# Kernel optimization log

Measured on AMD Instinct MI355X. Metric: run time of the kernel, lower is better.

## Reference

```python
import jax, jax.numpy as jnp
import numpy as np

N_NODES = 100000
N_GRAPHS = 256
EPS = 1e-5


def setup_inputs() -> dict:
    key = jax.random.key(0)
    ks = jax.random.split(key, 16)
    x = jax.random.normal(ks[0], (N_NODES, 7), dtype=jnp.float32)
    edge_index = jax.random.randint(ks[1], (2, 1600000), 0, N_NODES, dtype=jnp.int64)
    batch = jnp.sort(jax.random.randint(ks[2], (N_NODES,), 0, N_GRAPHS, dtype=jnp.int64))

    def lin(k, fi, fo):
        s = 1.0 / np.sqrt(fi)
        kw, kb = jax.random.split(k)
        W = jax.random.uniform(kw, (fi, fo), jnp.float32, -s, s)
        b = jax.random.uniform(kb, (fo,), jnp.float32, -s, s)
        return W, b

    W1, b1 = lin(ks[3], 7, 71)
    W2, b2 = lin(ks[4], 71, 135)
    W3, b3 = lin(ks[5], 135, 199)
    Wl1, bl1 = lin(ks[6], 199, 49)
    Wl2, bl2 = lin(ks[7], 49, 2)
    return {
        "x": x, "edge_index": edge_index, "batch": batch,
        "bn0_g": jnp.ones((7,)), "bn0_b": jnp.zeros((7,)),
        "bn1_g": jnp.ones((71,)), "bn1_b": jnp.zeros((71,)),
        "bn2_g": jnp.ones((135,)), "bn2_b": jnp.zeros((135,)),
        "W1": W1, "b1": b1, "W2": W2, "b2": b2, "W3": W3, "b3": b3,
        "Wl1": Wl1, "bl1": bl1, "Wl2": Wl2, "bl2": bl2,
    }


def _bn(x, g, b):
    # BatchNorm1d in training mode: batch stats over node dim
    m = jnp.mean(x, axis=0)
    v = jnp.mean(jnp.square(x - m), axis=0)
    return (x - m) * jax.lax.rsqrt(v + EPS) * g + b


def _gcn(x, src, dst, norm, W, b):
    # PyG GCNConv: x' = D^{-1/2} (A+I) D^{-1/2} (x W) + b
    h = x @ W
    out = jax.ops.segment_sum(norm[:, None] * h[src], dst, num_segments=N_NODES)
    return out + b


def reference(x, edge_index, batch, bn0_g, bn0_b, bn1_g, bn1_b, bn2_g, bn2_b,
              W1, b1, W2, b2, W3, b3, Wl1, bl1, Wl2, bl2):
    # add self loops
    loops = jnp.arange(N_NODES, dtype=edge_index.dtype)
    src = jnp.concatenate([edge_index[0], loops])
    dst = jnp.concatenate([edge_index[1], loops])
    deg = jax.ops.segment_sum(jnp.ones_like(dst, dtype=x.dtype), dst, num_segments=N_NODES)
    d_isqrt = jax.lax.rsqrt(jnp.maximum(deg, 1.0))
    norm = d_isqrt[src] * d_isqrt[dst]

    h = _bn(x, bn0_g, bn0_b)
    h = jax.nn.relu(_gcn(h, src, dst, norm, W1, b1))
    h = _bn(h, bn1_g, bn1_b)
    h = jax.nn.relu(_gcn(h, src, dst, norm, W2, b2))
    h = _bn(h, bn2_g, bn2_b)
    h = jax.nn.relu(_gcn(h, src, dst, norm, W3, b3))

    # global mean pool over graphs
    sums = jax.ops.segment_sum(h, batch, num_segments=N_GRAPHS)
    cnts = jax.ops.segment_sum(jnp.ones((h.shape[0],), h.dtype), batch, num_segments=N_GRAPHS)
    pooled = sums / jnp.maximum(cnts, 1.0)[:, None]

    out = pooled @ Wl1 + bl1
    out = out @ Wl2 + bl2
    return out
```

## Files before the change

### kernel.cpp

```cpp
#include <hip/hip_runtime.h>
#include <hip/hip_fp16.h>

#define EPSV 1e-5f
#define BIN_CH 4096
#define BCAP 8192

typedef _Float16 f16;
typedef f16 half8 __attribute__((ext_vector_type(8)));
typedef float f32x4 __attribute__((ext_vector_type(4)));


__global__ __launch_bounds__(256) void k_bin(const int* __restrict__ src,
                                             const int* __restrict__ dst, int E, int EN,
                                             int NBK, int* __restrict__ gcur,
                                             int* __restrict__ binned) {
    __shared__ int cnt[512];
    __shared__ int base[512];
    for (int b = threadIdx.x; b < 512; b += 256) cnt[b] = 0;
    __syncthreads();
    int i0 = blockIdx.x * BIN_CH;
    int i1 = i0 + BIN_CH; if (i1 > EN) i1 = EN;
    for (int i = i0 + threadIdx.x; i < i1; i += 256) {
        int d = (i < E) ? dst[i] : (i - E);
        atomicAdd(&cnt[d >> 8], 1);
    }
    __syncthreads();
    for (int b = threadIdx.x; b < NBK; b += 256)
        if (cnt[b]) base[b] = b * BCAP + atomicAdd(&gcur[b], cnt[b]);
    __syncthreads();
    for (int i = i0 + threadIdx.x; i < i1; i += 256) {
        int s, d;
        if (i < E) { s = src[i]; d = dst[i]; }
        else       { s = i - E; d = s; }
        int pos = atomicAdd(&base[d >> 8], 1);
        binned[pos] = s | ((d & 255) << 24);
    }
}

__global__ __launch_bounds__(256) void k_bucket(const int* __restrict__ binned,
                                                const int* __restrict__ gcur, int N,
                                                int* __restrict__ deg, int* __restrict__ rs,
                                                int* __restrict__ csr_s,
                                                float* __restrict__ disq) {
    __shared__ int deg_l[256];
    __shared__ int sc[256];
    __shared__ int cur_l[256];
    int b = blockIdx.x;
    int t = threadIdx.x;
    int start = b * BCAP, end = start + gcur[b];
    deg_l[t] = 0;
    __syncthreads();
    for (int i = start + t; i < end; i += 256)
        atomicAdd(&deg_l[((unsigned)binned[i]) >> 24], 1);
    __syncthreads();
    sc[t] = deg_l[t];
    __syncthreads();
    for (int off = 1; off < 256; off <<= 1) {
        int v = (t >= off) ? sc[t - off] : 0;
        __syncthreads();
        sc[t] += v;
        __syncthreads();
    }
    int rs_l = sc[t] - deg_l[t];
    int n = b * 256 + t;
    if (n < N) {
        deg[n] = deg_l[t];
        rs[n] = start + rs_l;
        disq[n] = rsqrtf((float)(deg_l[t] > 0 ? deg_l[t] : 1));
    }
    cur_l[t] = start + rs_l;
    __syncthreads();
    for (int i = start + t; i < end; i += 256) {
        int p = binned[i];
        int loc = ((unsigned)p) >> 24;
        int idx = atomicAdd(&cur_l[loc], 1);
        csr_s[idx] = p & 0xFFFFFF;
    }
}

__global__ __launch_bounds__(256) void k_wfill(const int* __restrict__ rs,
                                               const int* __restrict__ deg,
                                               const int* __restrict__ csr_s,
                                               const float* __restrict__ disq,
                                               float* __restrict__ csr_w, int N) {
    int wave = threadIdx.x >> 6, lane = threadIdx.x & 63;
    int n = blockIdx.x * 4 + wave;
    if (n >= N) return;
    int e0 = rs[n], dg = deg[n];
    float dn = disq[n];
    for (int j = lane; j < dg; j += 64) {
        int s = csr_s[e0 + j];
        csr_w[e0 + j] = disq[s] * dn;
    }
}


__global__ __launch_bounds__(256) void k_prep(
    const float* __restrict__ colsum, const float* __restrict__ colsq,
    const float* __restrict__ g, const float* __restrict__ b, float invN,
    const float* __restrict__ W, int Cin, int Cout, int KP,
    f16* __restrict__ Wp, float* __restrict__ wrow) {
    __shared__ float lsc[192];
    __shared__ float lsh[192];
    __shared__ float red[4];
    int t = threadIdx.x;
    int c = blockIdx.x;
    if (t < KP) {
        float scv = 0.f, shv = 0.f;
        if (t < Cin) {
            float m = colsum[t] * invN;
            float v = colsq[t] * invN - m * m;
            float rstd = rsqrtf(fmaxf(v, 0.f) + EPSV);
            scv = rstd * g[t];
            shv = b[t] - m * scv;
        }
        lsc[t] = scv; lsh[t] = shv;
    }
    __syncthreads();
    float part = 0.f;
    if (t < KP) {
        float wv = (t < Cin && c < Cout) ? W[(size_t)t * Cout + c] : 0.f;
        Wp[(size_t)c * KP + t] = (f16)(lsc[t] * wv);
        part = lsh[t] * wv;
    }
    for (int off = 32; off > 0; off >>= 1) part += __shfl_down(part, off);
    int lane = t & 63, wid = t >> 6;
    if (lane == 0) red[wid] = part;
    __syncthreads();
    if (t == 0) wrow[c] = red[0] + red[1] + red[2] + red[3];
}


__global__ __launch_bounds__(256) void k_padx_stats(const float* __restrict__ x,
                                                    __half* __restrict__ xp, int N,
                                                    float* __restrict__ colsum,
                                                    float* __restrict__ colsq) {
    __shared__ float ls[16];
    int t = threadIdx.x;
    int n = blockIdx.x * 256 + t;
    int lane = t & 63;
    if (t < 16) ls[t] = 0.f;
    __syncthreads();
    float v[7] = {0.f, 0.f, 0.f, 0.f, 0.f, 0.f, 0.f};
    if (n < N) {
#pragma unroll
        for (int j = 0; j < 7; ++j) v[j] = x[(size_t)n * 7 + j];
        __half h[8];
#pragma unroll
        for (int j = 0; j < 7; ++j) h[j] = __float2half(v[j]);
        h[7] = __float2half(0.f);
        *(float4*)(xp + (size_t)n * 8) = *(float4*)h;
    }
#pragma unroll
    for (int j = 0; j < 7; ++j) {
        float s = v[j];
        float q = v[j] * v[j];
        for (int off = 32; off > 0; off >>= 1) {
            s += __shfl_down(s, off);
            q += __shfl_down(q, off);
        }
        if (lane == 0) {
            atomicAdd(&ls[j], s);
            atomicAdd(&ls[8 + j], q);
        }
    }
    __syncthreads();
    if (t < 8)               atomicAdd(&colsum[t], ls[t]);
    else if (t < 16)         atomicAdd(&colsq[t - 8], ls[t]);
}


__global__ void k_gather8(const __half* __restrict__ xp, const int* __restrict__ csr_s,
                          const float* __restrict__ csr_w,
                          const int* __restrict__ rs, const int* __restrict__ deg,
                          __half* __restrict__ out, float* __restrict__ rsum, int N) {
    int n = blockIdx.x * blockDim.x + threadIdx.x;
    if (n >= N) return;
    int e0 = rs[n], eend = e0 + deg[n];
    float a0 = 0.f, a1 = 0.f, a2 = 0.f, a3 = 0.f, a4 = 0.f, a5 = 0.f, a6 = 0.f, a7 = 0.f;
    float ws = 0.f;
    for (int e = e0; e < eend; ++e) {
        int s = csr_s[e];
        float w = csr_w[e];
        ws += w;
        float4 r = *(const float4*)(xp + (size_t)s * 8);
        const __half2* hh = (const __half2*)&r;
        float2 q0 = __half22float2(hh[0]);
        float2 q1 = __half22float2(hh[1]);
        float2 q2 = __half22float2(hh[2]);
        float2 q3 = __half22float2(hh[3]);
        a0 = fmaf(w, q0.x, a0); a1 = fmaf(w, q0.y, a1);
        a2 = fmaf(w, q1.x, a2); a3 = fmaf(w, q1.y, a3);
        a4 = fmaf(w, q2.x, a4); a5 = fmaf(w, q2.y, a5);
        a6 = fmaf(w, q3.x, a6); a7 = fmaf(w, q3.y, a7);
    }
    rsum[n] = ws;
    __half h[8];
    h[0] = __float2half(a0); h[1] = __float2half(a1);
    h[2] = __float2half(a2); h[3] = __float2half(a3);
    h[4] = __float2half(a4); h[5] = __float2half(a5);
    h[6] = __float2half(a6); h[7] = __float2half(a7);
    *(float4*)(out + (size_t)n * 8) = *(float4*)h;
}

__global__ __launch_bounds__(256) void k_gather_w(
    const __half* __restrict__ Am, int SPm, const __half* __restrict__ At,
    int CH8, int NPW,
    const int* __restrict__ rs, const int* __restrict__ deg,
    const int* __restrict__ csr_s, const float* __restrict__ csr_w,
    __half* __restrict__ out, int SPo, int N) {
    int wave = threadIdx.x >> 6;
    int lane = threadIdx.x & 63;
    int sub = lane / CH8;
    int lsub = lane - sub * CH8;
    int n = (blockIdx.x * 4 + wave) * NPW + sub;
    bool active = (sub < NPW) && (n < N);
    int e0 = 0, eend = 0;
    if (active) { e0 = rs[n]; eend = e0 + deg[n]; }
    bool istail = (lsub == CH8 - 1);
    const __half* base = istail ? At : (Am + lsub * 8);
    const int stride = istail ? 8 : SPm;
    float acc[8] = {};

    int e = e0;
    for (; e + 8 <= eend; e += 8) {
        int s[8]; float wv[8]; float4 r[8];
#pragma unroll
        for (int i = 0; i < 8; ++i) { s[i] = csr_s[e + i]; wv[i] = csr_w[e + i]; }
#pragma unroll
        for (int i = 0; i < 8; ++i) r[i] = *(const float4*)(base + (size_t)(s[i] * stride));
#pragma unroll
        for (int i = 0; i < 8; ++i) {
            float2 q0 = __half22float2(((const __half2*)&r[i])[0]);
            float2 q1 = __half22float2(((const __half2*)&r[i])[1]);
            float2 q2 = __half22float2(((const __half2*)&r[i])[2]);
            float2 q3 = __half22float2(((const __half2*)&r[i])[3]);
            acc[0] = fmaf(wv[i], q0.x, acc[0]); acc[1] = fmaf(wv[i], q0.y, acc[1]);
            acc[2] = fmaf(wv[i], q1.x, acc[2]); acc[3] = fmaf(wv[i], q1.y, acc[3]);
            acc[4] = fmaf(wv[i], q2.x, acc[4]); acc[5] = fmaf(wv[i], q2.y, acc[5]);
            acc[6] = fmaf(wv[i], q3.x, acc[6]); acc[7] = fmaf(wv[i], q3.y, acc[7]);
        }
    }
    for (; e + 4 <= eend; e += 4) {
        int s[4]; float wv[4]; float4 r[4];
#pragma unroll
        for (int i = 0; i < 4; ++i) { s[i] = csr_s[e + i]; wv[i] = csr_w[e + i]; }
#pragma unroll
        for (int i = 0; i < 4; ++i) r[i] = *(const float4*)(base + (size_t)(s[i] * stride));
#pragma unroll
        for (int i = 0; i < 4; ++i) {
            float2 q0 = __half22float2(((const __half2*)&r[i])[0]);
            float2 q1 = __half22float2(((const __half2*)&r[i])[1]);
            float2 q2 = __half22float2(((const __half2*)&r[i])[2]);
            float2 q3 = __half22float2(((const __half2*)&r[i])[3]);
            acc[0] = fmaf(wv[i], q0.x, acc[0]); acc[1] = fmaf(wv[i], q0.y, acc[1]);
            acc[2] = fmaf(wv[i], q1.x, acc[2]); acc[3] = fmaf(wv[i], q1.y, acc[3]);
            acc[4] = fmaf(wv[i], q2.x, acc[4]); acc[5] = fmaf(wv[i], q2.y, acc[5]);
            acc[6] = fmaf(wv[i], q3.x, acc[6]); acc[7] = fmaf(wv[i], q3.y, acc[7]);
        }
    }
    for (; e < eend; ++e) {
        int s = csr_s[e];
        float w = csr_w[e];
        float4 r = *(const float4*)(base + (size_t)(s * stride));
        float2 q0 = __half22float2(((const __half2*)&r)[0]);
        float2 q1 = __half22float2(((const __half2*)&r)[1]);
        float2 q2 = __half22float2(((const __half2*)&r)[2]);
        float2 q3 = __half22float2(((const __half2*)&r)[3]);
        acc[0] = fmaf(w, q0.x, acc[0]); acc[1] = fmaf(w, q0.y, acc[1]);
        acc[2] = fmaf(w, q1.x, acc[2]); acc[3] = fmaf(w, q1.y, acc[3]);
        acc[4] = fmaf(w, q2.x, acc[4]); acc[5] = fmaf(w, q2.y, acc[5]);
        acc[6] = fmaf(w, q3.x, acc[6]); acc[7] = fmaf(w, q3.y, acc[7]);
    }

    if (active) {
        __half2 h[4];
        h[0] = __floats2half2_rn(acc[0], acc[1]);
        h[1] = __floats2half2_rn(acc[2], acc[3]);
        h[2] = __floats2half2_rn(acc[4], acc[5]);
        h[3] = __floats2half2_rn(acc[6], acc[7]);
        *(float4*)(out + (size_t)n * SPo + lsub * 8) = *(float4*)h;
    }
}


__global__ __launch_bounds__(256) void k_gemm_mfma(
    const f16* __restrict__ A, int SPa,
    const f16* __restrict__ Bt, int KP,
    const float* __restrict__ rsum, const float* __restrict__ wrow,
    const float* __restrict__ bias,
    f16* __restrict__ outM, int SPm, int MAIN, f16* __restrict__ outT, int TOTW,
    float* __restrict__ colsum, float* __restrict__ colsq, int do_stats,
    int N, int Cout) {
    __shared__ f16 As[128][40];
    __shared__ float s_sum[64];
    __shared__ float s_sq[64];
    const int r0 = blockIdx.x * 128;
    const int c0 = blockIdx.y * 64;
    const int t = threadIdx.x;
    const int wave = t >> 6, lane = t & 63;
    const int l15 = lane & 15, quad = lane >> 4;

    if (t < 64) { s_sum[t] = 0.f; s_sq[t] = 0.f; }

    f32x4 zero4 = {0.f, 0.f, 0.f, 0.f};
    f32x4 acc[2][4];
#pragma unroll
    for (int mi = 0; mi < 2; ++mi)
#pragma unroll
        for (int ni = 0; ni < 4; ++ni) acc[mi][ni] = zero4;

    const int KT = KP >> 5;
    for (int kt = 0; kt < KT; ++kt) {
        int k0 = kt * 32;
        {
            int kcol = (t & 7) * 4;
            int rbase = t >> 3;
            int gk = k0 + kcol;
            bool kok = (gk + 4 <= SPa);
#pragma unroll
            for (int i = 0; i < 4; ++i) {
                int row = rbase + i * 32;
                int gr = r0 + row;
                ushort4 v = {0, 0, 0, 0};
                if (gr < N && kok)
                    v = *(const ushort4*)(A + (size_t)gr * SPa + gk);
                *(ushort4*)&As[row][kcol] = v;
            }
        }
        __syncthreads();
        half8 a0 = *(const half8*)&As[wave * 32 + l15][quad * 8];
        half8 a1 = *(const half8*)&As[wave * 32 + 16 + l15][quad * 8];
#pragma unroll
        for (int ni = 0; ni < 4; ++ni) {
            half8 b = *(const half8*)(Bt + (size_t)(c0 + ni * 16 + l15) * KP + k0 + quad * 8);
            acc[0][ni] = __builtin_amdgcn_mfma_f32_16x16x32_f16(a0, b, acc[0][ni], 0, 0, 0);
            acc[1][ni] = __builtin_amdgcn_mfma_f32_16x16x32_f16(a1, b, acc[1][ni], 0, 0, 0);
        }
        __syncthreads();
    }

    float wr[4], bi[4];
#pragma unroll
    for (int ni = 0; ni < 4; ++ni) {
        int gc = c0 + ni * 16 + l15;
        wr[ni] = wrow[gc];
        bi[ni] = (gc < Cout) ? bias[gc] : 0.f;
    }
    float ps[4] = {}, pq[4] = {};
#pragma unroll
    for (int mi = 0; mi < 2; ++mi) {
#pragma unroll
        for (int reg = 0; reg < 4; ++reg) {
            int gr = r0 + wave * 32 + mi * 16 + quad * 4 + reg;
            if (gr >= N) continue;
            float rsv = rsum[gr];
#pragma unroll
            for (int ni = 0; ni < 4; ++ni) {
                int gc = c0 + ni * 16 + l15;
                float o = acc[mi][ni][reg] + rsv * wr[ni] + bi[ni];
                o = fmaxf(o, 0.f);
                if (gc >= Cout) o = 0.f;
                ps[ni] += o; pq[ni] += o * o;
                if (gc < MAIN) {
                    if (gc < TOTW) outM[(size_t)gr * SPm + gc] = (f16)o;
                } else if (gc < TOTW) {
                    outT[(size_t)gr * 8 + (gc - MAIN)] = (f16)o;
                }
            }
        }
    }
    if (do_stats) {
#pragma unroll
        for (int ni = 0; ni < 4; ++ni) {
            int cl = ni * 16 + l15;
            atomicAdd(&s_sum[cl], ps[ni]);
            atomicAdd(&s_sq[cl], pq[ni]);
        }
        __syncthreads();
        if (t < 64 && c0 + t < Cout) {
            atomicAdd(&colsum[c0 + t], s_sum[t]);
            atomicAdd(&colsq[c0 + t], s_sq[t]);
        }
    }
}


__global__ void k_pool_h(const __half* __restrict__ H, int SP, const int* __restrict__ batch,
                         int N, int C, float* __restrict__ pooled,
                         int* __restrict__ gstart, int* __restrict__ gend) {
    __shared__ int sb[128];
    int r0 = blockIdx.x * 128;
    int rows = N - r0; if (rows > 128) rows = 128;
    int t = threadIdx.x;
    if (t < rows) sb[t] = batch[r0 + t];
    __syncthreads();
    if (t < rows) {
        int n = r0 + t, g = sb[t];
        int prev = (n == 0) ? -1 : ((t == 0) ? batch[n - 1] : sb[t - 1]);
        if (prev != g) gstart[g] = n;
        int nxt = (n == N - 1) ? -1 : ((t == rows - 1) ? batch[n + 1] : sb[t + 1]);
        if (nxt != g) gend[g] = n + 1;
    }
    int c = t;
    if (c >= C) return;
    int cg = sb[0];
    float acc = 0.f;
    for (int r = 0; r < rows; ++r) {
        int g = sb[r];
        if (g != cg) { atomicAdd(&pooled[cg * C + c], acc); acc = 0.f; cg = g; }
        acc += __half2float(H[(size_t)(r0 + r) * SP + c]);
    }
    atomicAdd(&pooled[cg * C + c], acc);
}


__global__ void k_mlp(const float* __restrict__ pooled, const int* __restrict__ gstart,
                      const int* __restrict__ gend,
                      const float* __restrict__ Wl1, const float* __restrict__ bl1,
                      const float* __restrict__ Wl2, const float* __restrict__ bl2,
                      float* __restrict__ out, int C) {
    __shared__ float p[199];
    __shared__ float t1[49];
    int g = blockIdx.x;
    int cnt = gend[g] - gstart[g];
    float inv = 1.f / (float)(cnt > 1 ? cnt : 1);
    for (int k = threadIdx.x; k < C; k += blockDim.x) p[k] = pooled[g * C + k] * inv;
    __syncthreads();
    if (threadIdx.x < 49) {
        float acc = bl1[threadIdx.x];
        for (int k = 0; k < C; ++k) acc += p[k] * Wl1[k * 49 + threadIdx.x];
        t1[threadIdx.x] = acc;
    }
    __syncthreads();
    if (threadIdx.x < 2) {
        float acc = bl2[threadIdx.x];
        for (int k = 0; k < 49; ++k) acc += t1[k] * Wl2[k * 2 + threadIdx.x];
        out[g * 2 + threadIdx.x] = acc;
    }
}


extern "C" void kernel_launch(void* const* d_in, const int* in_sizes, int n_in,
                              void* d_out, int out_size, void* d_ws, size_t ws_size,
                              hipStream_t stream) {
    const float* x     = (const float*)d_in[0];
    const int*   ei    = (const int*)d_in[1];
    const int*   batch = (const int*)d_in[2];
    const float* bn0g = (const float*)d_in[3];
    const float* bn0b = (const float*)d_in[4];
    const float* bn1g = (const float*)d_in[5];
    const float* bn1b = (const float*)d_in[6];
    const float* bn2g = (const float*)d_in[7];
    const float* bn2b = (const float*)d_in[8];
    const float* W1  = (const float*)d_in[9];
    const float* b1  = (const float*)d_in[10];
    const float* W2  = (const float*)d_in[11];
    const float* b2  = (const float*)d_in[12];
    const float* W3  = (const float*)d_in[13];
    const float* b3  = (const float*)d_in[14];
    const float* Wl1 = (const float*)d_in[15];
    const float* bl1 = (const float*)d_in[16];
    const float* Wl2 = (const float*)d_in[17];
    const float* bl2 = (const float*)d_in[18];

    const int N = in_sizes[0] / 7;
    const int E = in_sizes[1] / 2;
    const int EN = E + N;
    const int G = out_size / 2;
    const int NB = (N + 255) / 256;
    const int NBK = (N + 255) / 256;
    const int NBIN = (EN + BIN_CH - 1) / BIN_CH;

    const int* src = ei;
    const int* dst = ei + E;

    char* w = (char*)d_ws;
    auto alloc = [&](size_t bytes) -> void* {
        void* p = (void*)w;
        w += ((bytes + 255) / 256) * 256;
        return p;
    };
    size_t szH1m = (size_t)N * 64 * sizeof(__half);
    size_t szH1t = (size_t)N * 8 * sizeof(__half);
    size_t szH2m = (size_t)N * 128 * sizeof(__half);
    size_t szH2t = (size_t)N * 8 * sizeof(__half);
    char* regA = (char*)alloc(szH1m + szH1t + szH2m + szH2t);
    __half* H1m = (__half*)regA;
    __half* H1t = (__half*)(regA + szH1m);
    __half* H2m = (__half*)(regA + szH1m + szH1t);
    __half* H2t = (__half*)(regA + szH1m + szH1t + szH2m);
    __half* H3  = (__half*)regA;

    __half* bufG = (__half*)alloc((size_t)N * 136 * sizeof(__half));
    f16*    wp   = (f16*)  alloc((size_t)256 * 160 * sizeof(f16));
    float*  wrow = (float*)alloc(256 * sizeof(float));
    __half* xp   = (__half*)alloc((size_t)N * 8 * sizeof(__half));
    float* disq  = (float*)alloc((size_t)N * sizeof(float));
    float* rsum  = (float*)alloc((size_t)N * sizeof(float));
    int*   deg   = (int*)  alloc((size_t)N * sizeof(int));
    int*   rs    = (int*)  alloc((size_t)N * sizeof(int));
    int*   binned= (int*)  alloc((size_t)NBK * BCAP * sizeof(int));
    int*   csr_s = (int*)  alloc((size_t)NBK * BCAP * sizeof(int));
    float* csr_w = (float*)alloc((size_t)NBK * BCAP * sizeof(float));
    float* colsum0 = (float*)alloc(256 * sizeof(float));
    float* colsq0  = (float*)alloc(256 * sizeof(float));
    float* colsumA = (float*)alloc(256 * sizeof(float));
    float* colsqA  = (float*)alloc(256 * sizeof(float));
    float* colsumB = (float*)alloc(256 * sizeof(float));
    float* colsqB  = (float*)alloc(256 * sizeof(float));
    int*   gcur    = (int*)  alloc(512 * sizeof(int));
    float* pooled  = (float*)alloc((size_t)G * 199 * sizeof(float));
    int*   gstart  = (int*)  alloc((size_t)G * sizeof(int));
    int*   gend    = (int*)  alloc((size_t)G * sizeof(int));

    size_t zbytes = 6 * 1024 + 2048 + (((size_t)G * 199 * sizeof(float) + 255) / 256) * 256;
    hipMemsetAsync(colsum0, 0, zbytes, stream);

    k_bin<<<NBIN, 256, 0, stream>>>(src, dst, E, EN, NBK, gcur, binned);
    k_bucket<<<NBK, 256, 0, stream>>>(binned, gcur, N, deg, rs, csr_s, disq);
    k_wfill<<<(N + 3) / 4, 256, 0, stream>>>(rs, deg, csr_s, disq, csr_w, N);

    const int GB = (N + 127) / 128;

    k_padx_stats<<<NB, 256, 0, stream>>>(x, xp, N, colsum0, colsq0);
    k_prep<<<128, 256, 0, stream>>>(colsum0, colsq0, bn0g, bn0b, 1.f / (float)N,
                                    W1, 7, 71, 32, wp, wrow);
    k_gather8<<<(N + 255) / 256, 256, 0, stream>>>(xp, csr_s, csr_w, rs, deg, bufG, rsum, N);
    {
        dim3 grid(GB, 2);
        k_gemm_mfma<<<grid, 256, 0, stream>>>((const f16*)bufG, 8, wp, 32, rsum, wrow, b1,
                                              (f16*)H1m, 64, 64, (f16*)H1t, 72,
                                              colsumA, colsqA, 1, N, 71);
    }
    k_prep<<<192, 256, 0, stream>>>(colsumA, colsqA, bn1g, bn1b, 1.f / (float)N,
                                    W2, 71, 135, 96, wp, wrow);
    k_gather_w<<<(N + 27) / 28, 256, 0, stream>>>(H1m, 64, H1t, 9, 7,
                                                  rs, deg, csr_s, csr_w, bufG, 72, N);
    {
        dim3 grid(GB, 3);
        k_gemm_mfma<<<grid, 256, 0, stream>>>((const f16*)bufG, 72, wp, 96, rsum, wrow, b2,
                                              (f16*)H2m, 128, 128, (f16*)H2t, 136,
                                              colsumB, colsqB, 1, N, 135);
    }
    k_prep<<<256, 256, 0, stream>>>(colsumB, colsqB, bn2g, bn2b, 1.f / (float)N,
                                    W3, 135, 199, 160, wp, wrow);
    k_gather_w<<<(N + 11) / 12, 256, 0, stream>>>(H2m, 128, H2t, 17, 3,
                                                  rs, deg, csr_s, csr_w, bufG, 136, N);
    {
        dim3 grid(GB, 4);
        k_gemm_mfma<<<grid, 256, 0, stream>>>((const f16*)bufG, 136, wp, 160, rsum, wrow, b3,
                                              (f16*)H3, 200, 256, (f16*)nullptr, 200,
                                              colsumB, colsqB, 0, N, 199);
    }

    k_pool_h<<<(N + 127) / 128, 256, 0, stream>>>(H3, 200, batch, N, 199, pooled, gstart, gend);
    k_mlp<<<G, 64, 0, stream>>>(pooled, gstart, gend, Wl1, bl1, Wl2, bl2, (float*)d_out, 199);
}
```

Before: 530.9 us.

## Fuse final GCN GEMM with mean pooling and split tail gather into separate kernel

The last GEMM now writes its ReLU outputs straight into per-graph pooled sums, using shared-memory accumulation for up to 16 graphs per tile. This removes the H3 store and the separate pooling kernel. The graph start/end detection moves into the input stats kernel. The gather kernel drops its divergent tail-lane path so lanes map by power-of-two shifts, and the 8-channel tail columns are handled by a new per-node kernel. The cost is an extra launch per layer and atomic contention in the pooling epilogue.

Result: slower. 600.4 us (+13.1%).

```diff
diff --git a/kernel.cpp b/kernel.cpp
--- a/kernel.cpp
+++ b/kernel.cpp
@@ -134,7 +134,10 @@
 __global__ __launch_bounds__(256) void k_padx_stats(const float* __restrict__ x,
                                                     __half* __restrict__ xp, int N,
                                                     float* __restrict__ colsum,
-                                                    float* __restrict__ colsq) {
+                                                    float* __restrict__ colsq,
+                                                    const int* __restrict__ batch,
+                                                    int* __restrict__ gstart,
+                                                    int* __restrict__ gend) {
     __shared__ float ls[16];
     int t = threadIdx.x;
     int n = blockIdx.x * 256 + t;
@@ -150,6 +153,11 @@
         for (int j = 0; j < 7; ++j) h[j] = __float2half(v[j]);
         h[7] = __float2half(0.f);
         *(float4*)(xp + (size_t)n * 8) = *(float4*)h;
+        int g = batch[n];
+        int gp = (n == 0) ? -1 : batch[n - 1];
+        if (gp != g) gstart[g] = n;
+        int gn = (n == N - 1) ? -1 : batch[n + 1];
+        if (gn != g) gend[g] = n + 1;
     }
 #pragma unroll
     for (int j = 0; j < 7; ++j) {
@@ -203,23 +211,51 @@
     *(float4*)(out + (size_t)n * 8) = *(float4*)h;
 }
 
+__global__ __launch_bounds__(256) void k_gather_tail(
+    const __half* __restrict__ At, const int* __restrict__ csr_s,
+    const float* __restrict__ csr_w, const int* __restrict__ rs,
+    const int* __restrict__ deg, __half* __restrict__ out, int SPo, int coff, int N) {
+    int n = blockIdx.x * blockDim.x + threadIdx.x;
+    if (n >= N) return;
+    int e0 = rs[n], eend = e0 + deg[n];
+    float a0 = 0.f, a1 = 0.f, a2 = 0.f, a3 = 0.f, a4 = 0.f, a5 = 0.f, a6 = 0.f, a7 = 0.f;
+    for (int e = e0; e < eend; ++e) {
+        int s = csr_s[e];
+        float w = csr_w[e];
+        float4 r = *(const float4*)(At + (size_t)s * 8);
+        const __half2* hh = (const __half2*)&r;
+        float2 q0 = __half22float2(hh[0]);
+        float2 q1 = __half22float2(hh[1]);
+        float2 q2 = __half22float2(hh[2]);
+        float2 q3 = __half22float2(hh[3]);
+        a0 = fmaf(w, q0.x, a0); a1 = fmaf(w, q0.y, a1);
+        a2 = fmaf(w, q1.x, a2); a3 = fmaf(w, q1.y, a3);
+        a4 = fmaf(w, q2.x, a4); a5 = fmaf(w, q2.y, a5);
+        a6 = fmaf(w, q3.x, a6); a7 = fmaf(w, q3.y, a7);
+    }
+    __half2 h[4];
+    h[0] = __floats2half2_rn(a0, a1);
+    h[1] = __floats2half2_rn(a2, a3);
+    h[2] = __floats2half2_rn(a4, a5);
+    h[3] = __floats2half2_rn(a6, a7);
+    *(float4*)(out + (size_t)n * SPo + coff) = *(float4*)h;
+}
+
 __global__ __launch_bounds__(256) void k_gather_w(
-    const __half* __restrict__ Am, int SPm, const __half* __restrict__ At,
-    int CH8, int NPW,
+    const __half* __restrict__ Am, int SPm, int SH,
     const int* __restrict__ rs, const int* __restrict__ deg,
     const int* __restrict__ csr_s, const float* __restrict__ csr_w,
     __half* __restrict__ out, int SPo, int N) {
     int wave = threadIdx.x >> 6;
     int lane = threadIdx.x & 63;
-    int sub = lane / CH8;
-    int lsub = lane - sub * CH8;
-    int n = (blockIdx.x * 4 + wave) * NPW + sub;
-    bool active = (sub < NPW) && (n < N);
+    int sub = lane >> SH;
+    int lsub = lane & ((1 << SH) - 1);
+    int npw = 64 >> SH;
+    int n = (blockIdx.x * 4 + wave) * npw + sub;
+    bool active = (n < N);
     int e0 = 0, eend = 0;
     if (active) { e0 = rs[n]; eend = e0 + deg[n]; }
-    bool istail = (lsub == CH8 - 1);
-    const __half* base = istail ? At : (Am + lsub * 8);
-    const int stride = istail ? 8 : SPm;
+    const __half* base = Am + lsub * 8;
     float acc[8] = {};
 
     int e = e0;
@@ -228,7 +264,7 @@
 #pragma unroll
         for (int i = 0; i < 8; ++i) { s[i] = csr_s[e + i]; wv[i] = csr_w[e + i]; }
 #pragma unroll
-        for (int i = 0; i < 8; ++i) r[i] = *(const float4*)(base + (size_t)(s[i] * stride));
+        for (int i = 0; i < 8; ++i) r[i] = *(const float4*)(base + (size_t)s[i] * SPm);
 #pragma unroll
         for (int i = 0; i < 8; ++i) {
             float2 q0 = __half22float2(((const __half2*)&r[i])[0]);
@@ -246,7 +282,7 @@
 #pragma unroll
         for (int i = 0; i < 4; ++i) { s[i] = csr_s[e + i]; wv[i] = csr_w[e + i]; }
 #pragma unroll
-        for (int i = 0; i < 4; ++i) r[i] = *(const float4*)(base + (size_t)(s[i] * stride));
+        for (int i = 0; i < 4; ++i) r[i] = *(const float4*)(base + (size_t)s[i] * SPm);
 #pragma unroll
         for (int i = 0; i < 4; ++i) {
             float2 q0 = __half22float2(((const __half2*)&r[i])[0]);
@@ -262,7 +298,7 @@
     for (; e < eend; ++e) {
         int s = csr_s[e];
         float w = csr_w[e];
-        float4 r = *(const float4*)(base + (size_t)(s * stride));
+        float4 r = *(const float4*)(base + (size_t)s * SPm);
         float2 q0 = __half22float2(((const __half2*)&r)[0]);
         float2 q1 = __half22float2(((const __half2*)&r)[1]);
         float2 q2 = __half22float2(((const __half2*)&r)[2]);
@@ -386,32 +422,106 @@
 }
 
 
-__global__ void k_pool_h(const __half* __restrict__ H, int SP, const int* __restrict__ batch,
-                         int N, int C, float* __restrict__ pooled,
-                         int* __restrict__ gstart, int* __restrict__ gend) {
-    __shared__ int sb[128];
-    int r0 = blockIdx.x * 128;
-    int rows = N - r0; if (rows > 128) rows = 128;
-    int t = threadIdx.x;
-    if (t < rows) sb[t] = batch[r0 + t];
-    __syncthreads();
-    if (t < rows) {
-        int n = r0 + t, g = sb[t];
-        int prev = (n == 0) ? -1 : ((t == 0) ? batch[n - 1] : sb[t - 1]);
-        if (prev != g) gstart[g] = n;
-        int nxt = (n == N - 1) ? -1 : ((t == rows - 1) ? batch[n + 1] : sb[t + 1]);
-        if (nxt != g) gend[g] = n + 1;
-    }
-    int c = t;
-    if (c >= C) return;
-    int cg = sb[0];
-    float acc = 0.f;
-    for (int r = 0; r < rows; ++r) {
-        int g = sb[r];
-        if (g != cg) { atomicAdd(&pooled[cg * C + c], acc); acc = 0.f; cg = g; }
-        acc += __half2float(H[(size_t)(r0 + r) * SP + c]);
-    }
-    atomicAdd(&pooled[cg * C + c], acc);
+__global__ __launch_bounds__(256) void k_gemm_pool(
+    const f16* __restrict__ A, int SPa,
+    const f16* __restrict__ Bt, int KP,
+    const float* __restrict__ rsum, const float* __restrict__ wrow,
+    const float* __restrict__ bias, const int* __restrict__ batch,
+    float* __restrict__ pooled, int N, int Cout) {
+    __shared__ f16 As[128][40];
+    __shared__ int sbat[128];
+    __shared__ float s_pool[16][64];
+    const int r0 = blockIdx.x * 128;
+    const int c0 = blockIdx.y * 64;
+    const int t = threadIdx.x;
+    const int wave = t >> 6, lane = t & 63;
+    const int l15 = lane & 15, quad = lane >> 4;
+
+    if (t < 128) {
+        int gr = r0 + t;
+        sbat[t] = batch[(gr < N) ? gr : (N - 1)];
+    }
+    for (int i = t; i < 16 * 64; i += 256) ((float*)s_pool)[i] = 0.f;
+
+    f32x4 zero4 = {0.f, 0.f, 0.f, 0.f};
+    f32x4 acc[2][4];
+#pragma unroll
+    for (int mi = 0; mi < 2; ++mi)
+#pragma unroll
+        for (int ni = 0; ni < 4; ++ni) acc[mi][ni] = zero4;
+
+    const int KT = KP >> 5;
+    for (int kt = 0; kt < KT; ++kt) {
+        int k0 = kt * 32;
+        {
+            int kcol = (t & 7) * 4;
+            int rbase = t >> 3;
+            int gk = k0 + kcol;
+            bool kok = (gk + 4 <= SPa);
+#pragma unroll
+            for (int i = 0; i < 4; ++i) {
+                int row = rbase + i * 32;
+                int gr = r0 + row;
+                ushort4 v = {0, 0, 0, 0};
+                if (gr < N && kok)
+                    v = *(const ushort4*)(A + (size_t)gr * SPa + gk);
+                *(ushort4*)&As[row][kcol] = v;
+            }
+        }
+        __syncthreads();
+        half8 a0 = *(const half8*)&As[wave * 32 + l15][quad * 8];
+        half8 a1 = *(const half8*)&As[wave * 32 + 16 + l15][quad * 8];
+#pragma unroll
+        for (int ni = 0; ni < 4; ++ni) {
+            half8 b = *(const half8*)(Bt + (size_t)(c0 + ni * 16 + l15) * KP + k0 + quad * 8);
+            acc[0][ni] = __builtin_amdgcn_mfma_f32_16x16x32_f16(a0, b, acc[0][ni], 0, 0, 0);
+            acc[1][ni] = __builtin_amdgcn_mfma_f32_16x16x32_f16(a1, b, acc[1][ni], 0, 0, 0);
+        }
+        __syncthreads();
+    }
+
+    const int g0 = sbat[0];
+    const int gmax = sbat[127];
+    float wr[4], bi[4];
+#pragma unroll
+    for (int ni = 0; ni < 4; ++ni) {
+        int gc = c0 + ni * 16 + l15;
+        wr[ni] = wrow[gc];
+        bi[ni] = (gc < Cout) ? bias[gc] : 0.f;
+    }
+#pragma unroll
+    for (int mi = 0; mi < 2; ++mi) {
+#pragma unroll
+        for (int reg = 0; reg < 4; ++reg) {
+            int lrow = wave * 32 + mi * 16 + quad * 4 + reg;
+            int gr = r0 + lrow;
+            if (gr >= N) continue;
+            float rsv = rsum[gr];
+            int slot = sbat[lrow] - g0;
+#pragma unroll
+            for (int ni = 0; ni < 4; ++ni) {
+                int gc = c0 + ni * 16 + l15;
+                if (gc >= Cout) continue;
+                float o = acc[mi][ni][reg] + rsv * wr[ni] + bi[ni];
+                o = fmaxf(o, 0.f);
+                if (slot < 16) atomicAdd(&s_pool[slot][ni * 16 + l15], o);
+                else           atomicAdd(&pooled[(size_t)(g0 + slot) * Cout + gc], o);
+            }
+        }
+    }
+    __syncthreads();
+    {
+        int cl = t & 63, sl = t >> 6;
+        int gc = c0 + cl;
+        if (gc < Cout) {
+            for (int slot = sl; slot < 16; slot += 4) {
+                int g = g0 + slot;
+                if (g > gmax) break;
+                float v = s_pool[slot][cl];
+                if (v != 0.f) atomicAdd(&pooled[(size_t)g * Cout + gc], v);
+            }
+        }
+    }
 }
 
 
@@ -490,7 +600,6 @@
     __half* H1t = (__half*)(regA + szH1m);
     __half* H2m = (__half*)(regA + szH1m + szH1t);
     __half* H2t = (__half*)(regA + szH1m + szH1t + szH2m);
-    __half* H3  = (__half*)regA;
 
     __half* bufG = (__half*)alloc((size_t)N * 136 * sizeof(__half));
     f16*    wp   = (f16*)  alloc((size_t)256 * 160 * sizeof(f16));
@@ -523,7 +632,7 @@
 
     const int GB = (N + 127) / 128;
 
-    k_padx_stats<<<NB, 256, 0, stream>>>(x, xp, N, colsum0, colsq0);
+    k_padx_stats<<<NB, 256, 0, stream>>>(x, xp, N, colsum0, colsq0, batch, gstart, gend);
     k_prep<<<128, 256, 0, stream>>>(colsum0, colsq0, bn0g, bn0b, 1.f / (float)N,
                                     W1, 7, 71, 32, wp, wrow);
     k_gather8<<<(N + 255) / 256, 256, 0, stream>>>(xp, csr_s, csr_w, rs, deg, bufG, rsum, N);
@@ -535,8 +644,10 @@
     }
     k_prep<<<192, 256, 0, stream>>>(colsumA, colsqA, bn1g, bn1b, 1.f / (float)N,
                                     W2, 71, 135, 96, wp, wrow);
-    k_gather_w<<<(N + 27) / 28, 256, 0, stream>>>(H1m, 64, H1t, 9, 7,
+    k_gather_w<<<(N + 31) / 32, 256, 0, stream>>>(H1m, 64, 3,
                                                   rs, deg, csr_s, csr_w, bufG, 72, N);
+    k_gather_tail<<<(N + 255) / 256, 256, 0, stream>>>(H1t, csr_s, csr_w, rs, deg,
+                                                       bufG, 72, 64, N);
     {
         dim3 grid(GB, 3);
         k_gemm_mfma<<<grid, 256, 0, stream>>>((const f16*)bufG, 72, wp, 96, rsum, wrow, b2,
@@ -545,15 +656,15 @@
     }
     k_prep<<<256, 256, 0, stream>>>(colsumB, colsqB, bn2g, bn2b, 1.f / (float)N,
                                     W3, 135, 199, 160, wp, wrow);
-    k_gather_w<<<(N + 11) / 12, 256, 0, stream>>>(H2m, 128, H2t, 17, 3,
+    k_gather_w<<<(N + 15) / 16, 256, 0, stream>>>(H2m, 128, 4,
                                                   rs, deg, csr_s, csr_w, bufG, 136, N);
+    k_gather_tail<<<(N + 255) / 256, 256, 0, stream>>>(H2t, csr_s, csr_w, rs, deg,
+                                                       bufG, 136, 128, N);
     {
         dim3 grid(GB, 4);
-        k_gemm_mfma<<<grid, 256, 0, stream>>>((const f16*)bufG, 136, wp, 160, rsum, wrow, b3,
-                                              (f16*)H3, 200, 256, (f16*)nullptr, 200,
-                                              colsumB, colsqB, 0, N, 199);
-    }
-
-    k_pool_h<<<(N + 127) / 128, 256, 0, stream>>>(H3, 200, batch, N, 199, pooled, gstart, gend);
+        k_gemm_pool<<<grid, 256, 0, stream>>>((const f16*)bufG, 136, wp, 160, rsum, wrow, b3,
+                                              batch, pooled, N, 199);
+    }
+
     k_mlp<<<G, 64, 0, stream>>>(pooled, gstart, gend, Wl1, bl1, Wl2, bl2, (float*)d_out, 199);
 }
```
